# Kernel optimization log

Measured on AMD Instinct MI355X. Metric: run time of the kernel, lower is better.

The kernel has to match this reference:

```python
import jax, jax.numpy as jnp
import numpy as np

B, D, NH, HD, L, P, FF = 2, 256, 8, 32, 4, 4, 1024
SPATIAL = np.array([[100, 100], [50, 50], [25, 25], [13, 13]], dtype=np.int64)
S_TOTAL = int(SPATIAL.prod(1).sum())  # 13294
EPS = 1e-5


def setup_inputs() -> dict:
    key = jax.random.key(0)
    ks = jax.random.split(key, 20)
    std = 0.02
    f32 = jnp.float32
    return {
        "query": jax.random.normal(ks[0], (B, S_TOTAL, D), f32),
        "query_pos": jax.random.normal(ks[1], (B, S_TOTAL, D), f32),
        "valid_ratios": jnp.ones((B, L, 2), f32),
        "spatial_shapes": SPATIAL,
        "level_start_index": np.concatenate([[0], SPATIAL.prod(1).cumsum()[:-1]]).astype(np.int64),
        "W_off": jax.random.normal(ks[2], (D, NH * L * P * 2), f32) * std,
        "b_off": jax.random.normal(ks[3], (NH * L * P * 2,), f32) * std,
        "W_attn": jax.random.normal(ks[4], (D, NH * L * P), f32) * std,
        "b_attn": jax.random.normal(ks[5], (NH * L * P,), f32) * std,
        "W_val": jax.random.normal(ks[6], (D, D), f32) * std,
        "b_val": jnp.zeros((D,), f32),
        "W_out": jax.random.normal(ks[7], (D, D), f32) * std,
        "b_out": jnp.zeros((D,), f32),
        "ln1_g": jnp.ones((D,), f32),
        "ln1_b": jnp.zeros((D,), f32),
        "W1": jax.random.normal(ks[8], (D, FF), f32) * std,
        "b1": jnp.zeros((FF,), f32),
        "W2": jax.random.normal(ks[9], (FF, D), f32) * std,
        "b2": jnp.zeros((D,), f32),
        "ln2_g": jnp.ones((D,), f32),
        "ln2_b": jnp.zeros((D,), f32),
    }


def _layer_norm(x, g, b):
    m = x.mean(-1, keepdims=True)
    v = ((x - m) ** 2).mean(-1, keepdims=True)
    return (x - m) * jax.lax.rsqrt(v + EPS) * g + b


def _bilinear_sample(v, loc, H, W):
    # v: [B, NH, H*W, HD]; loc: [B, NH, S, P, 2] normalized to [0,1]
    # Matches F.grid_sample(bilinear, padding_mode='zeros', align_corners=False)
    x = loc[..., 0] * W - 0.5
    y = loc[..., 1] * H - 0.5
    x0 = jnp.floor(x)
    y0 = jnp.floor(y)
    lx, ly = x - x0, y - y0
    x0i = x0.astype(jnp.int32)
    y0i = y0.astype(jnp.int32)
    x1i, y1i = x0i + 1, y0i + 1

    def corner(yi, xi, w):
        valid = (xi >= 0) & (xi < W) & (yi >= 0) & (yi < H)
        idx = jnp.clip(yi, 0, H - 1) * W + jnp.clip(xi, 0, W - 1)  # [B,NH,S,P]
        b_, h_, s_, p_ = idx.shape
        g = jnp.take_along_axis(v, idx.reshape(b_, h_, s_ * p_)[..., None], axis=2)
        g = g.reshape(b_, h_, s_, p_, -1)
        return g * (w * valid)[..., None]

    return (corner(y0i, x0i, (1 - lx) * (1 - ly)) + corner(y0i, x1i, lx * (1 - ly))
            + corner(y1i, x0i, (1 - lx) * ly) + corner(y1i, x1i, lx * ly))


def _forward(query, query_pos, valid_ratios, spatial_shapes,
             W_off, b_off, W_attn, b_attn, W_val, b_val, W_out, b_out,
             ln1_g, ln1_b, W1, b1, W2, b2, ln2_g, ln2_b):
    ss = np.asarray(spatial_shapes)
    Bq, S, _ = query.shape

    # ----- reference points (per-pixel centers, normalized by valid ratios) -----
    refs = []
    for lvl in range(ss.shape[0]):
        H, W = int(ss[lvl, 0]), int(ss[lvl, 1])
        ry, rx = jnp.meshgrid(jnp.linspace(0.5, H - 0.5, H), jnp.linspace(0.5, W - 0.5, W), indexing='ij')
        vy = valid_ratios[:, lvl, 1][:, None, None]
        vx = valid_ratios[:, lvl, 0][:, None, None]
        ry = ry[None] / (vy * H)
        rx = rx[None] / (vx * W)
        refs.append(jnp.stack((rx, ry), -1).reshape(Bq, H * W, 2))
    ref = jnp.concatenate(refs, 1)  # [B, S, 2] (identical across levels)

    # ----- multi-scale deformable attention -----
    q = query + query_pos
    v = (query @ W_val + b_val).reshape(Bq, S, NH, HD).transpose(0, 2, 1, 3)  # [B,NH,S,HD]
    off = (q @ W_off + b_off).reshape(Bq, S, NH, L, P, 2)
    aw = jax.nn.softmax((q @ W_attn + b_attn).reshape(Bq, S, NH, L * P), -1)
    aw = aw.reshape(Bq, S, NH, L, P)
    normalizer = jnp.asarray(ss[:, ::-1].copy(), jnp.float32)  # (W, H) per level
    loc = ref[:, :, None, None, None, :] + off / normalizer[None, None, None, :, None, :]  # [B,S,NH,L,P,2]

    starts = np.concatenate([[0], ss.prod(1).cumsum()[:-1]])
    out = jnp.zeros((Bq, NH, S, HD), query.dtype)
    for lvl in range(ss.shape[0]):
        H, W = int(ss[lvl, 0]), int(ss[lvl, 1])
        s0 = int(starts[lvl])
        v_l = v[:, :, s0:s0 + H * W]                       # [B,NH,HW,HD]
        loc_l = loc[:, :, :, lvl].transpose(0, 2, 1, 3, 4)  # [B,NH,S,P,2]
        samp = _bilinear_sample(v_l, loc_l, H, W)           # [B,NH,S,P,HD]
        w_l = aw[:, :, :, lvl].transpose(0, 2, 1, 3)        # [B,NH,S,P]
        out = out + (samp * w_l[..., None]).sum(3)
    attn_out = out.transpose(0, 2, 1, 3).reshape(Bq, S, D) @ W_out + b_out

    # ----- residual + LN + FFN + residual + LN -----
    x = _layer_norm(query + attn_out, ln1_g, ln1_b)
    f = jax.nn.relu(x @ W1 + b1) @ W2 + b2
    return _layer_norm(x + f, ln2_g, ln2_b)


def reference(query, query_pos, valid_ratios, spatial_shapes, level_start_index,
              W_off, b_off, W_attn, b_attn, W_val, b_val, W_out, b_out,
              ln1_g, ln1_b, W1, b1, W2, b2, ln2_g, ln2_b):
    return _forward(query, query_pos, valid_ratios, spatial_shapes,
                    W_off, b_off, W_attn, b_attn, W_val, b_val, W_out, b_out,
                    ln1_g, ln1_b, W1, b1, W2, b2, ln2_g, ln2_b)
```

## Files before the change

### kernel.cpp

```cpp
#include <hip/hip_runtime.h>
#include <math.h>

#define R_ROWS 26588
#define S_TOT  13294
#define NHEAD  8
#define NLVL   4
#define EPSF   1e-5f

typedef __attribute__((ext_vector_type(8))) short short8;
typedef __attribute__((ext_vector_type(4))) float f32x4;
typedef __attribute__((ext_vector_type(2))) float f32x2;
typedef unsigned short ushort_t;

__device__ __forceinline__ unsigned short f2bf(float f) {
    unsigned int u = __builtin_bit_cast(unsigned int, f);
    unsigned int r = (u + 0x7FFFu + ((u >> 16) & 1u)) >> 16;
    return (unsigned short)r;
}

__global__ __launch_bounds__(256) void prep_kernel(
    const float* __restrict__ W_val, const float* __restrict__ W_off,
    const float* __restrict__ W_attn, const float* __restrict__ W_out,
    const float* __restrict__ W1, const float* __restrict__ W2,
    ushort_t* __restrict__ wt_val, ushort_t* __restrict__ wt_off,
    ushort_t* __restrict__ wt_attn, ushort_t* __restrict__ wt_out,
    ushort_t* __restrict__ wt_w1, ushort_t* __restrict__ wt_w2,
    const float* __restrict__ query, const float* __restrict__ qpos,
    ushort_t* __restrict__ qry_bf, ushort_t* __restrict__ qsum_bf)
{
    __shared__ ushort_t tt[32][33];
    int bid = blockIdx.x;
    if (bid < 736) {
        const float* src; ushort_t* dst; int K, N, t;
        if (bid < 64)       { src = W_val;  dst = wt_val;  K = 256;  N = 256;  t = bid; }
        else if (bid < 128) { src = W_off;  dst = wt_off;  K = 256;  N = 256;  t = bid - 64; }
        else if (bid < 160) { src = W_attn; dst = wt_attn; K = 256;  N = 128;  t = bid - 128; }
        else if (bid < 224) { src = W_out;  dst = wt_out;  K = 256;  N = 256;  t = bid - 160; }
        else if (bid < 480) { src = W1;     dst = wt_w1;   K = 256;  N = 1024; t = bid - 224; }
        else                { src = W2;     dst = wt_w2;   K = 1024; N = 256;  t = bid - 480; }
        int nt = N / 32;
        int bn = (t % nt) * 32, bk = (t / nt) * 32;
        int x = threadIdx.x & 31;
        int y = threadIdx.x >> 5;
#pragma unroll
        for (int i = 0; i < 4; ++i) {
            int k = y + i * 8;
            tt[x][k] = f2bf(src[(long)(bk + k) * N + bn + x]);
        }
        __syncthreads();
#pragma unroll
        for (int i = 0; i < 4; ++i) {
            int n = y + i * 8;
            dst[(long)(bn + n) * K + bk + x] = tt[n][x];
        }
    } else {
        int i = (bid - 736) * 256 + threadIdx.x;
        float4 a = ((const float4*)query)[i];
        float4 b = ((const float4*)qpos)[i];
        uint2 qa, qs;
        qa.x = (unsigned)f2bf(a.x) | ((unsigned)f2bf(a.y) << 16);
        qa.y = (unsigned)f2bf(a.z) | ((unsigned)f2bf(a.w) << 16);
        qs.x = (unsigned)f2bf(a.x + b.x) | ((unsigned)f2bf(a.y + b.y) << 16);
        qs.y = (unsigned)f2bf(a.z + b.z) | ((unsigned)f2bf(a.w + b.w) << 16);
        ((uint2*)qry_bf)[i] = qa;
        ((uint2*)qsum_bf)[i] = qs;
    }
}

__device__ __forceinline__ void stage_ab(
    const ushort_t* __restrict__ Arow, const ushort_t* __restrict__ Brow,
    int K, int k0, ushort_t* As, ushort_t* Bs, int wave, int lane)
{
    int quadS = lane & 3;
    int rr = lane >> 2;
#pragma unroll
    for (int inst = 0; inst < 2; ++inst) {
        int base_row = wave * 32 + inst * 16;
        int r = base_row + rr;
        int quadG = quadS ^ ((r >> 1) & 3);
        const ushort_t* gp = Arow + (long)r * K + k0 + quadG * 8;
        __builtin_amdgcn_global_load_lds(
            (const __attribute__((address_space(1))) unsigned int*)gp,
            (__attribute__((address_space(3))) unsigned int*)&As[base_row * 32],
            16, 0, 0);
    }
#pragma unroll
    for (int inst = 0; inst < 2; ++inst) {
        int base_row = wave * 32 + inst * 16;
        int r = base_row + rr;
        int quadG = quadS ^ ((r >> 1) & 3);
        const ushort_t* gp = Brow + (long)r * K + k0 + quadG * 8;
        __builtin_amdgcn_global_load_lds(
            (const __attribute__((address_space(1))) unsigned int*)gp,
            (__attribute__((address_space(3))) unsigned int*)&Bs[base_row * 32],
            16, 0, 0);
    }
}

__device__ __forceinline__ void gemm_body(
    ushort_t* As, ushort_t* Bs,
    const ushort_t* __restrict__ A, const ushort_t* __restrict__ Wt,
    const float* __restrict__ bias, void* __restrict__ Cv,
    int M, int N, int K, int bm, int bn, bool out_bf16, bool relu)
{
    const int tid  = threadIdx.x;
    const int wave = tid >> 6;
    const int lane = tid & 63;
    const int l15  = lane & 15;
    const int quad = lane >> 4;
    const int wm   = (wave >> 1) * 64;
    const int wn   = (wave & 1) * 64;

    const ushort_t* Arow = A + (long)bm * K;
    const ushort_t* Brow = Wt + (long)bn * K;

    f32x4 acc[4][4];
#pragma unroll
    for (int i = 0; i < 4; ++i)
#pragma unroll
        for (int j = 0; j < 4; ++j) acc[i][j] = (f32x4)0.0f;

    int aoff[4], boff[4];
#pragma unroll
    for (int mi = 0; mi < 4; ++mi) {
        int r = wm + mi * 16 + l15;
        aoff[mi] = r * 32 + (quad ^ ((r >> 1) & 3)) * 8;
    }
#pragma unroll
    for (int ni = 0; ni < 4; ++ni) {
        int r = wn + ni * 16 + l15;
        boff[ni] = r * 32 + (quad ^ ((r >> 1) & 3)) * 8;
    }

    const int NT = K >> 5;
    stage_ab(Arow, Brow, K, 0,  As,        Bs,        wave, lane);
    stage_ab(Arow, Brow, K, 32, As + 4096, Bs + 4096, wave, lane);
    int cur = 0;
    for (int t = 0; t < NT; ++t) {
        if (t + 2 < NT) {
            int nb = cur + 2; if (nb >= 3) nb -= 3;
            stage_ab(Arow, Brow, K, (t + 2) << 5,
                     As + nb * 4096, Bs + nb * 4096, wave, lane);
            asm volatile("s_waitcnt vmcnt(8)" ::: "memory");
        } else if (t + 2 == NT) {
            asm volatile("s_waitcnt vmcnt(4)" ::: "memory");
        } else {
            asm volatile("s_waitcnt vmcnt(0)" ::: "memory");
        }
        asm volatile("s_barrier" ::: "memory");

        const ushort_t* Ab = As + cur * 4096;
        const ushort_t* Bb = Bs + cur * 4096;
        short8 af[4], bf[4];
#pragma unroll
        for (int mi = 0; mi < 4; ++mi) af[mi] = *(const short8*)&Ab[aoff[mi]];
#pragma unroll
        for (int ni = 0; ni < 4; ++ni) bf[ni] = *(const short8*)&Bb[boff[ni]];
#pragma unroll
        for (int mi = 0; mi < 4; ++mi)
#pragma unroll
            for (int ni = 0; ni < 4; ++ni)
                acc[mi][ni] = __builtin_amdgcn_mfma_f32_16x16x32_bf16(
                    af[mi], bf[ni], acc[mi][ni], 0, 0, 0);
        if (t + 3 < NT)
            asm volatile("s_barrier" ::: "memory");
        cur = cur + 1; if (cur >= 3) cur -= 3;
    }

#pragma unroll
    for (int mi = 0; mi < 4; ++mi) {
#pragma unroll
        for (int r = 0; r < 4; ++r) {
            int row = bm + wm + mi * 16 + quad * 4 + r;
            if (row >= M) continue;
#pragma unroll
            for (int ni = 0; ni < 4; ++ni) {
                int col = bn + wn + ni * 16 + l15;
                float vv = acc[mi][ni][r] + bias[col];
                if (relu) vv = fmaxf(vv, 0.f);
                if (out_bf16)
                    ((ushort_t*)Cv)[(long)row * N + col] = f2bf(vv);
                else
                    ((float*)Cv)[(long)row * N + col] = vv;
            }
        }
    }
}

template<bool OUT_BF16, bool RELU>
__global__ __launch_bounds__(256, 3) void gemm_mfma_kernel(
    const ushort_t* __restrict__ A, const ushort_t* __restrict__ Wt,
    const float* __restrict__ bias, void* __restrict__ Cv,
    int M, int N, int K)
{
    __shared__ ushort_t As[3 * 4096];
    __shared__ ushort_t Bs[3 * 4096];
    gemm_body(As, Bs, A, Wt, bias, Cv, M, N, K,
              blockIdx.x * 128, blockIdx.y * 128, OUT_BF16, RELU);
}

__global__ __launch_bounds__(256, 3) void proj_kernel(
    const ushort_t* __restrict__ qry_bf, const ushort_t* __restrict__ q_bf,
    const ushort_t* __restrict__ wt_val, const ushort_t* __restrict__ wt_off,
    const ushort_t* __restrict__ wt_attn,
    const float* __restrict__ b_val, const float* __restrict__ b_off,
    const float* __restrict__ b_attn,
    ushort_t* __restrict__ v_bf, float* __restrict__ cb, float* __restrict__ logits)
{
    __shared__ ushort_t As[3 * 4096];
    __shared__ ushort_t Bs[3 * 4096];
    int y = blockIdx.y;
    const ushort_t* A; const ushort_t* Wt; const float* bias;
    void* C; bool outbf; int N, bn;
    if (y < 2)      { A = qry_bf; Wt = wt_val;  bias = b_val;  C = v_bf;   outbf = true;  N = 256; bn = y * 128; }
    else if (y < 4) { A = q_bf;   Wt = wt_off;  bias = b_off;  C = cb;     outbf = false; N = 256; bn = (y - 2) * 128; }
    else            { A = q_bf;   Wt = wt_attn; bias = b_attn; C = logits; outbf = false; N = 128; bn = 0; }
    gemm_body(As, Bs, A, Wt, bias, C, R_ROWS, N, 256, blockIdx.x * 128, bn, outbf, false);
}

__device__ __forceinline__ void stage_ln64(
    const ushort_t* __restrict__ Arow, const ushort_t* __restrict__ Brow,
    int K, int k0, ushort_t* As, ushort_t* Bs, int wave, int lane)
{
    int quadS = lane & 3;
    int rr = lane >> 2;
    {
        int base_row = wave * 16;
        int r = base_row + rr;
        int quadG = quadS ^ ((r >> 1) & 3);
        const ushort_t* gp = Arow + (long)r * K + k0 + quadG * 8;
        __builtin_amdgcn_global_load_lds(
            (const __attribute__((address_space(1))) unsigned int*)gp,
            (__attribute__((address_space(3))) unsigned int*)&As[base_row * 32],
            16, 0, 0);
    }
#pragma unroll
    for (int inst = 0; inst < 4; ++inst) {
        int base_row = wave * 64 + inst * 16;
        int r = base_row + rr;
        int quadG = quadS ^ ((r >> 1) & 3);
        const ushort_t* gp = Brow + (long)r * K + k0 + quadG * 8;
        __builtin_amdgcn_global_load_lds(
            (const __attribute__((address_space(1))) unsigned int*)gp,
            (__attribute__((address_space(3))) unsigned int*)&Bs[base_row * 32],
            16, 0, 0);
    }
}

template<bool DUAL>
__global__ __launch_bounds__(256, 2) void gemm_ln_kernel(
    const ushort_t* __restrict__ A, const ushort_t* __restrict__ Wt,
    const float* __restrict__ bias, const float* __restrict__ resid,
    const float* __restrict__ gam, const float* __restrict__ bet,
    float* __restrict__ outf, ushort_t* __restrict__ outb,
    int M, int K)
{
    __shared__ ushort_t As[3 * 2048];
    __shared__ ushort_t Bs[3 * 8192];
    __shared__ float s1s[64][4], s2s[64][4];

    const int tid  = threadIdx.x;
    const int wave = tid >> 6;
    const int lane = tid & 63;
    const int l15  = lane & 15;
    const int quad = lane >> 4;
    const int wn   = wave * 64;
    const int bm   = blockIdx.x * 64;

    const ushort_t* Arow = A + (long)bm * K;

    float bias4[4], g4[4], be4[4];
#pragma unroll
    for (int ni = 0; ni < 4; ++ni) {
        int col = wn + ni * 16 + l15;
        bias4[ni] = bias[col];
        g4[ni]    = gam[col];
        be4[ni]   = bet[col];
    }
    float rv[4][4][4];
#pragma unroll
    for (int mi = 0; mi < 4; ++mi)
#pragma unroll
        for (int rr = 0; rr < 4; ++rr) {
            int row = bm + mi * 16 + quad * 4 + rr;
#pragma unroll
            for (int ni = 0; ni < 4; ++ni) {
                int col = wn + ni * 16 + l15;
                rv[mi][rr][ni] = (row < M) ? resid[(long)row * 256 + col] : 0.f;
            }
        }

    f32x4 acc[4][4];
#pragma unroll
    for (int i = 0; i < 4; ++i)
#pragma unroll
        for (int j = 0; j < 4; ++j) acc[i][j] = (f32x4)0.0f;

    int aoff[4], boff[4];
#pragma unroll
    for (int mi = 0; mi < 4; ++mi) {
        int r = mi * 16 + l15;
        aoff[mi] = r * 32 + (quad ^ ((r >> 1) & 3)) * 8;
    }
#pragma unroll
    for (int ni = 0; ni < 4; ++ni) {
        int r = wn + ni * 16 + l15;
        boff[ni] = r * 32 + (quad ^ ((r >> 1) & 3)) * 8;
    }

    const int NT = K >> 5;
    stage_ln64(Arow, Wt, K, 0, As, Bs, wave, lane);
    int cur = 0;
    for (int t = 0; t < NT; ++t) {
        int nxt = cur + 1; if (nxt == 3) nxt = 0;
        if (t + 1 < NT) {
            stage_ln64(Arow, Wt, K, (t + 1) << 5,
                       As + nxt * 2048, Bs + nxt * 8192, wave, lane);
            asm volatile("s_waitcnt vmcnt(5)" ::: "memory");
        } else {
            asm volatile("s_waitcnt vmcnt(0)" ::: "memory");
        }
        asm volatile("s_barrier" ::: "memory");

        const ushort_t* Ab = As + cur * 2048;
        const ushort_t* Bb = Bs + cur * 8192;
        short8 af[4], bf[4];
#pragma unroll
        for (int mi = 0; mi < 4; ++mi) af[mi] = *(const short8*)&Ab[aoff[mi]];
#pragma unroll
        for (int ni = 0; ni < 4; ++ni) bf[ni] = *(const short8*)&Bb[boff[ni]];
#pragma unroll
        for (int mi = 0; mi < 4; ++mi)
#pragma unroll
            for (int ni = 0; ni < 4; ++ni)
                acc[mi][ni] = __builtin_amdgcn_mfma_f32_16x16x32_bf16(
                    af[mi], bf[ni], acc[mi][ni], 0, 0, 0);
        cur = nxt;
    }

#pragma unroll
    for (int mi = 0; mi < 4; ++mi)
#pragma unroll
        for (int rr = 0; rr < 4; ++rr) {
            float s1 = 0.f, s2 = 0.f;
#pragma unroll
            for (int ni = 0; ni < 4; ++ni) {
                float x = acc[mi][ni][rr] + bias4[ni] + rv[mi][rr][ni];
                acc[mi][ni][rr] = x;
                s1 += x; s2 += x * x;
            }
#pragma unroll
            for (int o = 1; o < 16; o <<= 1) {
                s1 += __shfl_xor(s1, o);
                s2 += __shfl_xor(s2, o);
            }
            if (l15 == 0) {
                int rl = mi * 16 + quad * 4 + rr;
                s1s[rl][wave] = s1;
                s2s[rl][wave] = s2;
            }
        }
    __syncthreads();
#pragma unroll
    for (int mi = 0; mi < 4; ++mi)
#pragma unroll
        for (int rr = 0; rr < 4; ++rr) {
            int rl  = mi * 16 + quad * 4 + rr;
            int row = bm + rl;
            float t1 = s1s[rl][0] + s1s[rl][1] + s1s[rl][2] + s1s[rl][3];
            float t2 = s2s[rl][0] + s2s[rl][1] + s2s[rl][2] + s2s[rl][3];
            float mean = t1 * (1.f / 256.f);
            float var  = t2 * (1.f / 256.f) - mean * mean;
            float inv  = rsqrtf(var + EPSF);
            if (row < M) {
#pragma unroll
                for (int ni = 0; ni < 4; ++ni) {
                    int col = wn + ni * 16 + l15;
                    float y = (acc[mi][ni][rr] - mean) * inv * g4[ni] + be4[ni];
                    outf[(long)row * 256 + col] = y;
                    if (DUAL) outb[(long)row * 256 + col] = f2bf(y);
                }
            }
        }
}

#define DEF_BLOCKS 3328
#define DEF_CHUNK  416

__global__ __launch_bounds__(256, 4) void deform_sample_kernel(
    const ushort_t* __restrict__ v, const float* __restrict__ off,
    const float* __restrict__ logits, const float* __restrict__ vr,
    ushort_t* __restrict__ out)
{
    const int Hs_[4] = {100, 50, 25, 13};
    const int S0_[4] = {0, 10000, 12500, 13125};

    __shared__ float meta[64 * 132];

    int wb  = (blockIdx.x & 7) * DEF_CHUNK + (blockIdx.x >> 3);
    int grp = wb * 64 + (threadIdx.x >> 2);
    int j   = threadIdx.x & 3;
    if (grp >= R_ROWS * NHEAD) return;
    int h = grp & 7;
    int r = grp >> 3;
    int b = (r >= S_TOT) ? 1 : 0;
    int s = r - b * S_TOT;

    int lq = (s < 10000) ? 0 : (s < 12500) ? 1 : (s < 13125) ? 2 : 3;
    int t  = s - S0_[lq];
    int Wq = Hs_[lq];
    int iy = t / Wq;
    int jx = t - iy * Wq;
    float vx = vr[(b * NLVL + lq) * 2 + 0];
    float vy = vr[(b * NLVL + lq) * 2 + 1];
    float rx = (jx + 0.5f) / (vx * (float)Wq);
    float ry = (iy + 0.5f) / (vy * (float)Wq);

    const float* offp = off + (long)r * 256 + h * 32;
    float4 oa = ((const float4*)offp)[2 * j];
    float4 ob = ((const float4*)offp)[2 * j + 1];
    float4 lg = ((const float4*)(logits + (long)grp * 16))[j];

    float mx = fmaxf(fmaxf(lg.x, lg.y), fmaxf(lg.z, lg.w));
    mx = fmaxf(mx, __shfl_xor(mx, 1));
    mx = fmaxf(mx, __shfl_xor(mx, 2));
    float e0 = __expf(lg.x - mx), e1 = __expf(lg.y - mx);
    float e2 = __expf(lg.z - mx), e3 = __expf(lg.w - mx);
    float sum = e0 + e1 + e2 + e3;
    sum += __shfl_xor(sum, 1);
    sum += __shfl_xor(sum, 2);
    float inv = 1.f / sum;

    const int   H  = Hs_[j];
    const float fH = (float)H;
    const int   s0 = S0_[j];
    const int   boff = b ? (S_TOT * 512) : 0;
    float oxs[4] = {oa.x, oa.z, ob.x, ob.z};
    float oys[4] = {oa.y, oa.w, ob.y, ob.w};
    float wts[4] = {e0 * inv, e1 * inv, e2 * inv, e3 * inv};

    float* mg = &meta[(threadIdx.x >> 2) * 132];
#pragma unroll
    for (int i = 0; i < 4; ++i) {
        float x = rx * fH + oxs[i] - 0.5f;
        float y = ry * fH + oys[i] - 0.5f;
        float xf = floorf(x), yf = floorf(y);
        float lx = x - xf, ly = y - yf;
        int x0 = (int)xf, y0 = (int)yf;
        bool xv0 = (x0 >= 0) & (x0 < H);
        bool xv1 = (x0 >= -1) & (x0 < H - 1);
        bool yv0 = (y0 >= 0) & (y0 < H);
        bool yv1 = (y0 >= -1) & (y0 < H - 1);
        float w = wts[i];
        f32x4 w4;
        w4.x = (xv0 & yv0) ? (1.f - lx) * (1.f - ly) * w : 0.f;
        w4.y = (xv1 & yv0) ? lx * (1.f - ly) * w : 0.f;
        w4.z = (xv0 & yv1) ? (1.f - lx) * ly * w : 0.f;
        w4.w = (xv1 & yv1) ? lx * ly * w : 0.f;
        int xc0 = min(max(x0, 0), H - 1), xc1 = min(max(x0 + 1, 0), H - 1);
        int yc0 = min(max(y0, 0), H - 1), yc1 = min(max(y0 + 1, 0), H - 1);
        int4 o4;
        o4.x = ((s0 + yc0 * H + xc0) << 9) + boff;
        o4.y = ((s0 + yc0 * H + xc1) << 9) + boff;
        o4.z = ((s0 + yc1 * H + xc0) << 9) + boff;
        o4.w = ((s0 + yc1 * H + xc1) << 9) + boff;
        int pt = i * 4 + j;
        *(f32x4*)&mg[pt * 8]     = w4;
        *(int4*) &mg[pt * 8 + 4] = o4;
    }
    asm volatile("s_waitcnt lgkmcnt(0)" ::: "memory");

    const char* vbase = (const char*)v;
    const unsigned loff = (unsigned)(h * 64 + j * 16);
    f32x2 acc2[4];
#pragma unroll
    for (int c = 0; c < 4; ++c) acc2[c] = (f32x2)0.0f;

#define FMA4(G, WGT) do {                                                    \
        unsigned uu0 = (G).x, uu1 = (G).y, uu2 = (G).z, uu3 = (G).w;         \
        f32x2 gv;                                                            \
        gv.x = __builtin_bit_cast(float, uu0 << 16);                         \
        gv.y = __builtin_bit_cast(float, uu0 & 0xFFFF0000u);                 \
        acc2[0] += gv * (WGT);                                               \
        gv.x = __builtin_bit_cast(float, uu1 << 16);                         \
        gv.y = __builtin_bit_cast(float, uu1 & 0xFFFF0000u);                 \
        acc2[1] += gv * (WGT);                                               \
        gv.x = __builtin_bit_cast(float, uu2 << 16);                         \
        gv.y = __builtin_bit_cast(float, uu2 & 0xFFFF0000u);                 \
        acc2[2] += gv * (WGT);                                               \
        gv.x = __builtin_bit_cast(float, uu3 << 16);                         \
        gv.y = __builtin_bit_cast(float, uu3 & 0xFFFF0000u);                 \
        acc2[3] += gv * (WGT);                                               \
    } while (0)

#pragma unroll
    for (int pp = 0; pp < 8; ++pp) {
        f32x4 wA = *(const f32x4*)&mg[(2 * pp) * 8];
        int4  oA = *(const int4*) &mg[(2 * pp) * 8 + 4];
        f32x4 wB = *(const f32x4*)&mg[(2 * pp + 1) * 8];
        int4  oB = *(const int4*) &mg[(2 * pp + 1) * 8 + 4];
        uint4 gA0 = *(const uint4*)(vbase + ((unsigned)oA.x + loff));
        uint4 gA1 = *(const uint4*)(vbase + ((unsigned)oA.y + loff));
        uint4 gA2 = *(const uint4*)(vbase + ((unsigned)oA.z + loff));
        uint4 gA3 = *(const uint4*)(vbase + ((unsigned)oA.w + loff));
        uint4 gB0 = *(const uint4*)(vbase + ((unsigned)oB.x + loff));
        uint4 gB1 = *(const uint4*)(vbase + ((unsigned)oB.y + loff));
        uint4 gB2 = *(const uint4*)(vbase + ((unsigned)oB.z + loff));
        uint4 gB3 = *(const uint4*)(vbase + ((unsigned)oB.w + loff));
        FMA4(gA0, wA.x); FMA4(gA1, wA.y); FMA4(gA2, wA.z); FMA4(gA3, wA.w);
        FMA4(gB0, wB.x); FMA4(gB1, wB.y); FMA4(gB2, wB.z); FMA4(gB3, wB.w);
    }
#undef FMA4

    uint4 o;
    o.x = (unsigned)f2bf(acc2[0].x) | ((unsigned)f2bf(acc2[0].y) << 16);
    o.y = (unsigned)f2bf(acc2[1].x) | ((unsigned)f2bf(acc2[1].y) << 16);
    o.z = (unsigned)f2bf(acc2[2].x) | ((unsigned)f2bf(acc2[2].y) << 16);
    o.w = (unsigned)f2bf(acc2[3].x) | ((unsigned)f2bf(acc2[3].y) << 16);
    *(uint4*)&out[(long)r * 256 + h * 32 + j * 8] = o;
}

extern "C" void kernel_launch(void* const* d_in, const int* in_sizes, int n_in,
                              void* d_out, int out_size, void* d_ws, size_t ws_size,
                              hipStream_t stream)
{
    const float* query  = (const float*)d_in[0];
    const float* qpos   = (const float*)d_in[1];
    const float* vr     = (const float*)d_in[2];
    const float* W_off  = (const float*)d_in[5];
    const float* b_off  = (const float*)d_in[6];
    const float* W_attn = (const float*)d_in[7];
    const float* b_attn = (const float*)d_in[8];
    const float* W_val  = (const float*)d_in[9];
    const float* b_val  = (const float*)d_in[10];
    const float* W_out  = (const float*)d_in[11];
    const float* b_out  = (const float*)d_in[12];
    const float* ln1g   = (const float*)d_in[13];
    const float* ln1b   = (const float*)d_in[14];
    const float* W1     = (const float*)d_in[15];
    const float* b1     = (const float*)d_in[16];
    const float* W2     = (const float*)d_in[17];
    const float* b2     = (const float*)d_in[18];
    const float* ln2g   = (const float*)d_in[19];
    const float* ln2b   = (const float*)d_in[20];
    float* out = (float*)d_out;

    float* ws = (float*)d_ws;
    const long R128 = (long)R_ROWS * 128;
    ushort_t* q_bf    = (ushort_t*)(ws);
    ushort_t* qry_bf  = (ushort_t*)(ws + R128);
    ushort_t* v_bf    = (ushort_t*)(ws + 2 * R128);
    float*    logits  = ws + 3 * R128;
    ushort_t* h_bf    = (ushort_t*)(ws);
    float*    cb      = ws + 4 * R128;
    ushort_t* samp_bf = (ushort_t*)(ws + 6 * R128);
    float*    xb      = ws + 7 * R128;
    ushort_t* wt      = (ushort_t*)(ws + 9 * R128);
    ushort_t* wt_val  = wt;
    ushort_t* wt_off  = wt + 65536;
    ushort_t* wt_attn = wt + 131072;
    ushort_t* wt_out  = wt + 163840;
    ushort_t* wt_w1   = wt + 229376;
    ushort_t* wt_w2   = wt + 491520;

    dim3 blk(256);
    const int MB128 = (R_ROWS + 127) / 128;
    const int MB64  = (R_ROWS + 63) / 64;

    prep_kernel<<<736 + R_ROWS / 4, blk, 0, stream>>>(
        W_val, W_off, W_attn, W_out, W1, W2,
        wt_val, wt_off, wt_attn, wt_out, wt_w1, wt_w2,
        query, qpos, qry_bf, q_bf);
    proj_kernel<<<dim3(MB128, 5), blk, 0, stream>>>(
        qry_bf, q_bf, wt_val, wt_off, wt_attn, b_val, b_off, b_attn,
        v_bf, cb, logits);
    deform_sample_kernel<<<DEF_BLOCKS, blk, 0, stream>>>(
        v_bf, cb, logits, vr, samp_bf);
    gemm_ln_kernel<true><<<MB64, blk, 0, stream>>>(
        samp_bf, wt_out, b_out, query, ln1g, ln1b, xb, samp_bf, R_ROWS, 256);
    gemm_mfma_kernel<true, true><<<dim3(MB128, 8), blk, 0, stream>>>(
        samp_bf, wt_w1, b1, h_bf, R_ROWS, 1024, 256);
    gemm_ln_kernel<false><<<MB64, blk, 0, stream>>>(
        h_bf, wt_w2, b2, xb, ln2g, ln2b, out, nullptr, R_ROWS, 1024);
}
```

Measured before the change: 291.8 us.

## Split deformable sampling points across two thread halves with shuffle reduction

Each (row, head) group now uses 8 threads instead of 4, with two halves each handling two of the four sampling points per level. The partial bilinear accumulations are combined with a cross-lane shuffle and only one half writes the output. The block count doubles, shared metadata per block halves, and launch bounds rise to 6 waves per SIMD. The aim is more memory-level parallelism and occupancy for the latency-bound gathers, at the cost of extra shuffles, redundant softmax and coordinate work, and idle lanes during the store.

```diff
diff --git a/kernel.cpp b/kernel.cpp
--- a/kernel.cpp
+++ b/kernel.cpp
@@ -384,10 +384,9 @@
         }
 }
 
-#define DEF_BLOCKS 3328
-#define DEF_CHUNK  416
-
-__global__ __launch_bounds__(256, 4) void deform_sample_kernel(
+#define DEF_BLOCKS 6647
+
+__global__ __launch_bounds__(256, 6) void deform_sample_kernel(
     const ushort_t* __restrict__ v, const float* __restrict__ off,
     const float* __restrict__ logits, const float* __restrict__ vr,
     ushort_t* __restrict__ out)
@@ -395,11 +394,13 @@
     const int Hs_[4] = {100, 50, 25, 13};
     const int S0_[4] = {0, 10000, 12500, 13125};
 
-    __shared__ float meta[64 * 132];
-
-    int wb  = (blockIdx.x & 7) * DEF_CHUNK + (blockIdx.x >> 3);
-    int grp = wb * 64 + (threadIdx.x >> 2);
-    int j   = threadIdx.x & 3;
+    __shared__ float meta[32 * 132];
+
+    int bid = blockIdx.x;
+    int wb  = (bid & 7) * 831 + (bid >> 3);
+    int grp = wb * 32 + (threadIdx.x >> 3);
+    int j    = threadIdx.x & 3;
+    int half = (threadIdx.x >> 2) & 1;
     if (grp >= R_ROWS * NHEAD) return;
     int h = grp & 7;
     int r = grp >> 3;
@@ -417,17 +418,18 @@
     float ry = (iy + 0.5f) / (vy * (float)Wq);
 
     const float* offp = off + (long)r * 256 + h * 32;
-    float4 oa = ((const float4*)offp)[2 * j];
-    float4 ob = ((const float4*)offp)[2 * j + 1];
+    float4 op = ((const float4*)offp)[2 * j + half];
     float4 lg = ((const float4*)(logits + (long)grp * 16))[j];
 
     float mx = fmaxf(fmaxf(lg.x, lg.y), fmaxf(lg.z, lg.w));
     mx = fmaxf(mx, __shfl_xor(mx, 1));
     mx = fmaxf(mx, __shfl_xor(mx, 2));
-    float e0 = __expf(lg.x - mx), e1 = __expf(lg.y - mx);
-    float e2 = __expf(lg.z - mx), e3 = __expf(lg.w - mx);
-    float sum = e0 + e1 + e2 + e3;
-    sum += __shfl_xor(sum, 1);
+    float l0 = half ? lg.z : lg.x;
+    float l1 = half ? lg.w : lg.y;
+    float e0 = __expf(l0 - mx), e1 = __expf(l1 - mx);
+    float sl = e0 + e1;
+    float s4 = sl + __shfl_xor(sl, 4);
+    float sum = s4 + __shfl_xor(s4, 1);
     sum += __shfl_xor(sum, 2);
     float inv = 1.f / sum;
 
@@ -435,15 +437,15 @@
     const float fH = (float)H;
     const int   s0 = S0_[j];
     const int   boff = b ? (S_TOT * 512) : 0;
-    float oxs[4] = {oa.x, oa.z, ob.x, ob.z};
-    float oys[4] = {oa.y, oa.w, ob.y, ob.w};
-    float wts[4] = {e0 * inv, e1 * inv, e2 * inv, e3 * inv};
-
-    float* mg = &meta[(threadIdx.x >> 2) * 132];
-#pragma unroll
-    for (int i = 0; i < 4; ++i) {
-        float x = rx * fH + oxs[i] - 0.5f;
-        float y = ry * fH + oys[i] - 0.5f;
+    float oxs2[2] = {op.x, op.z};
+    float oys2[2] = {op.y, op.w};
+    float wts2[2] = {e0 * inv, e1 * inv};
+
+    float* mg = &meta[(threadIdx.x >> 3) * 132];
+#pragma unroll
+    for (int ii = 0; ii < 2; ++ii) {
+        float x = rx * fH + oxs2[ii] - 0.5f;
+        float y = ry * fH + oys2[ii] - 0.5f;
         float xf = floorf(x), yf = floorf(y);
         float lx = x - xf, ly = y - yf;
         int x0 = (int)xf, y0 = (int)yf;
@@ -451,7 +453,7 @@
         bool xv1 = (x0 >= -1) & (x0 < H - 1);
         bool yv0 = (y0 >= 0) & (y0 < H);
         bool yv1 = (y0 >= -1) & (y0 < H - 1);
-        float w = wts[i];
+        float w = wts2[ii];
         f32x4 w4;
         w4.x = (xv0 & yv0) ? (1.f - lx) * (1.f - ly) * w : 0.f;
         w4.y = (xv1 & yv0) ? lx * (1.f - ly) * w : 0.f;
@@ -464,7 +466,7 @@
         o4.y = ((s0 + yc0 * H + xc1) << 9) + boff;
         o4.z = ((s0 + yc1 * H + xc0) << 9) + boff;
         o4.w = ((s0 + yc1 * H + xc1) << 9) + boff;
-        int pt = i * 4 + j;
+        int pt = 8 * half + 4 * ii + j;
         *(f32x4*)&mg[pt * 8]     = w4;
         *(int4*) &mg[pt * 8 + 4] = o4;
     }
@@ -493,31 +495,32 @@
         acc2[3] += gv * (WGT);                                               \
     } while (0)
 
-#pragma unroll
-    for (int pp = 0; pp < 8; ++pp) {
-        f32x4 wA = *(const f32x4*)&mg[(2 * pp) * 8];
-        int4  oA = *(const int4*) &mg[(2 * pp) * 8 + 4];
-        f32x4 wB = *(const f32x4*)&mg[(2 * pp + 1) * 8];
-        int4  oB = *(const int4*) &mg[(2 * pp + 1) * 8 + 4];
-        uint4 gA0 = *(const uint4*)(vbase + ((unsigned)oA.x + loff));
-        uint4 gA1 = *(const uint4*)(vbase + ((unsigned)oA.y + loff));
-        uint4 gA2 = *(const uint4*)(vbase + ((unsigned)oA.z + loff));
-        uint4 gA3 = *(const uint4*)(vbase + ((unsigned)oA.w + loff));
-        uint4 gB0 = *(const uint4*)(vbase + ((unsigned)oB.x + loff));
-        uint4 gB1 = *(const uint4*)(vbase + ((unsigned)oB.y + loff));
-        uint4 gB2 = *(const uint4*)(vbase + ((unsigned)oB.z + loff));
-        uint4 gB3 = *(const uint4*)(vbase + ((unsigned)oB.w + loff));
-        FMA4(gA0, wA.x); FMA4(gA1, wA.y); FMA4(gA2, wA.z); FMA4(gA3, wA.w);
-        FMA4(gB0, wB.x); FMA4(gB1, wB.y); FMA4(gB2, wB.z); FMA4(gB3, wB.w);
+    const float* ms = &mg[half * 64];
+#pragma unroll
+    for (int m = 0; m < 8; ++m) {
+        f32x4 w4 = *(const f32x4*)&ms[m * 8];
+        int4  o4 = *(const int4*) &ms[m * 8 + 4];
+        uint4 g0 = *(const uint4*)(vbase + ((unsigned)o4.x + loff));
+        uint4 g1 = *(const uint4*)(vbase + ((unsigned)o4.y + loff));
+        uint4 g2 = *(const uint4*)(vbase + ((unsigned)o4.z + loff));
+        uint4 g3 = *(const uint4*)(vbase + ((unsigned)o4.w + loff));
+        FMA4(g0, w4.x); FMA4(g1, w4.y); FMA4(g2, w4.z); FMA4(g3, w4.w);
     }
 #undef FMA4
 
-    uint4 o;
-    o.x = (unsigned)f2bf(acc2[0].x) | ((unsigned)f2bf(acc2[0].y) << 16);
-    o.y = (unsigned)f2bf(acc2[1].x) | ((unsigned)f2bf(acc2[1].y) << 16);
-    o.z = (unsigned)f2bf(acc2[2].x) | ((unsigned)f2bf(acc2[2].y) << 16);
-    o.w = (unsigned)f2bf(acc2[3].x) | ((unsigned)f2bf(acc2[3].y) << 16);
-    *(uint4*)&out[(long)r * 256 + h * 32 + j * 8] = o;
+#pragma unroll
+    for (int c = 0; c < 4; ++c) {
+        acc2[c].x += __shfl_xor(acc2[c].x, 4);
+        acc2[c].y += __shfl_xor(acc2[c].y, 4);
+    }
+    if (half == 0) {
+        uint4 o;
+        o.x = (unsigned)f2bf(acc2[0].x) | ((unsigned)f2bf(acc2[0].y) << 16);
+        o.y = (unsigned)f2bf(acc2[1].x) | ((unsigned)f2bf(acc2[1].y) << 16);
+        o.z = (unsigned)f2bf(acc2[2].x) | ((unsigned)f2bf(acc2[2].y) << 16);
+        o.w = (unsigned)f2bf(acc2[3].x) | ((unsigned)f2bf(acc2[3].y) << 16);
+        *(uint4*)&out[(long)r * 256 + h * 32 + j * 8] = o;
+    }
 }
 
 extern "C" void kernel_launch(void* const* d_in, const int* in_sizes, int n_in,
```

Result: no change. 290.9 us (median of 2 runs) (-0.3%).
